# Performance work log

Measured on AMD Instinct MI355X. Metric: run time of the kernel, lower is better.

## Reference

```python
import jax, jax.numpy as jnp
import numpy as np

B, S, D = 4, 2048, 1024      # batch, seq, d_model
H = 4096                     # expert hidden_size
E, K = 8, 2                  # num_experts, top_k
Z_COEF, BAL_COEF = 0.001, 0.01


def setup_inputs() -> dict:
    key = jax.random.key(0)
    ks = jax.random.split(key, 10)
    sc = 0.02
    return {
        "x": jax.random.normal(ks[0], (B, S, D), jnp.float32),
        "gate_w": jax.random.normal(ks[1], (D, E), jnp.float32) * sc,
        "keys_w": jax.random.normal(ks[2], (E, D, H), jnp.float32) * sc,
        "keys_b": jnp.zeros((E, H), jnp.float32),
        "values_w": jax.random.normal(ks[3], (E, H, D), jnp.float32) * sc,
        "values_b": jnp.zeros((E, D), jnp.float32),
        "shared_keys_w": jax.random.normal(ks[4], (D, H), jnp.float32) * sc,
        "shared_keys_b": jnp.zeros((H,), jnp.float32),
        "shared_values_w": jax.random.normal(ks[5], (H, D), jnp.float32) * sc,
        "shared_values_b": jnp.zeros((D,), jnp.float32),
    }


def reference(x, gate_w, keys_w, keys_b, values_w, values_b,
              shared_keys_w, shared_keys_b, shared_values_w, shared_values_b):
    b, s, d = x.shape
    xf = x.reshape(-1, d)                                  # [N, D]

    # ---- Router (top-k, softmax over selected scores) ----
    logits = xf @ gate_w                                   # [N, E]
    scores, idx = jax.lax.top_k(logits, K)                 # [N, K]
    w = jax.nn.softmax(scores, axis=-1)                    # [N, K]

    # Aux losses (training path)
    one_hot = jax.nn.one_hot(idx, E, dtype=w.dtype)        # [N, K, E]
    usage = (one_hot * w[..., None]).sum(axis=(0, 1))      # [E]
    balance_loss = usage.std() / usage.mean() * BAL_COEF
    z_loss = jnp.square(jax.nn.logsumexp(logits, axis=-1)).mean() * Z_COEF
    router_loss = balance_loss + z_loss

    # ---- Shared expert(s): single FFN, divided by count (=1) ----
    out = jax.nn.gelu(xf @ shared_keys_w + shared_keys_b) @ shared_values_w + shared_values_b

    # ---- Training path: dense per-expert FFN, masked combine ----
    # hidden: [N, E, H]
    hidden = jax.nn.gelu(jnp.einsum('nd,edh->neh', xf, keys_w) + keys_b)
    expert_out = jnp.einsum('neh,ehd->ned', hidden, values_w) + values_b  # [N, E, D]
    comb = (one_hot * w[..., None]).sum(axis=1)            # [N, E] per-token expert weight
    out = out + jnp.einsum('ned,ne->nd', expert_out, comb)

    return out.reshape(b, s, d), router_loss
```

## Files before the change

kernel.cpp:

```cpp
#include <hip/hip_runtime.h>
#include <hip/hip_bf16.h>


#define N_TOK 8192
#define DM    1024
#define HD    4096
#define NE    8
#define NKTOT 16384
#define PERM_CAP 17408
#define MAX_TILES 136
#define BAND 17
#define EV_BLOCKS 1088
#define RTOK_BLK 16

typedef __attribute__((ext_vector_type(8))) short bhalf8;
typedef __attribute__((ext_vector_type(8))) unsigned short ushort8v;
typedef __attribute__((ext_vector_type(4))) float floatx4;

__device__ __forceinline__ unsigned short f2bf(float f) {
  union { float f; unsigned int u; } v; v.f = f;
  unsigned int u = v.u;
  return (unsigned short)((u + 0x7fffu + ((u >> 16) & 1u)) >> 16);
}

__device__ __forceinline__ float bf2f(unsigned short h) {
  union { unsigned int u; float f; } v; v.u = ((unsigned int)h) << 16;
  return v.f;
}

__device__ __forceinline__ float gelu_tanh(float h) {
  float u = 0.7978845608028654f * (h + 0.044715f * h * h * h);
  float t = 1.0f - 2.0f / (1.0f + __expf(2.0f * u));
  return 0.5f * h * (1.0f + t);
}

__device__ __forceinline__ void gload16(const unsigned short* g, void* l) {
  __builtin_amdgcn_global_load_lds(
      (const __attribute__((address_space(1))) void*)g,
      (__attribute__((address_space(3))) void*)l, 16, 0, 0);
}

__global__ void init_cvt_kernel(const float* __restrict__ x, unsigned short* __restrict__ xb,
                                int* perm, float* permw, float* usage, float* zsum,
                                int* counts, int* fill) {
  int b = blockIdx.x;
  int i = b * 256 + threadIdx.x;
  size_t ci = (size_t)i * 4;
  float4 v = *(const float4*)(x + ci);
  ushort4 o;
  o.x = f2bf(v.x); o.y = f2bf(v.y); o.z = f2bf(v.z); o.w = f2bf(v.w);
  *(ushort4*)(xb + ci) = o;
  if (i < PERM_CAP) { perm[i] = 0; permw[i] = 0.0f; }
  if (i < NE) { usage[i] = 0.0f; counts[i] = 0; fill[i] = 0; }
  if (i == 0) zsum[0] = 0.0f;
}

__global__ void router_kernel(const float* __restrict__ x, const float* __restrict__ gw,
                              int* __restrict__ idxb, float* __restrict__ wbuf,
                              float* __restrict__ usage, float* __restrict__ zsum,
                              int* __restrict__ counts) {
  __shared__ float s_use[NE];
  __shared__ int   s_cnt[NE];
  __shared__ float s_z;
  int t = threadIdx.x;
  if (t < NE) { s_use[t] = 0.0f; s_cnt[t] = 0; }
  if (t == 0) s_z = 0.0f;
  __syncthreads();

  int wave = t >> 6;
  int lane = t & 63;

  float luse[NE]; int lcnt[NE];
#pragma unroll
  for (int e = 0; e < NE; e++) { luse[e] = 0.0f; lcnt[e] = 0; }
  float lz = 0.0f;

#pragma unroll
  for (int i = 0; i < 4; i++) {
    int n = blockIdx.x * RTOK_BLK + wave * 4 + i;
    const float* xr = x + (size_t)n * DM;
    float acc[NE];
#pragma unroll
    for (int e = 0; e < NE; e++) acc[e] = 0.0f;
    for (int d = lane; d < DM; d += 64) {
      float xv = xr[d];
      const float* g = gw + (size_t)d * NE;
#pragma unroll
      for (int e = 0; e < NE; e++) acc[e] += xv * g[e];
    }
#pragma unroll
    for (int e = 0; e < NE; e++) {
#pragma unroll
      for (int off = 32; off > 0; off >>= 1) acc[e] += __shfl_xor(acc[e], off);
    }
    if (lane == 0) {
      float m1 = acc[0]; int i1 = 0;
#pragma unroll
      for (int e = 1; e < NE; e++) if (acc[e] > m1) { m1 = acc[e]; i1 = e; }
      float m2 = -3.0e38f; int i2 = 0;
#pragma unroll
      for (int e = 0; e < NE; e++) if (e != i1 && acc[e] > m2) { m2 = acc[e]; i2 = e; }
      float e1 = __expf(m2 - m1);
      float w1 = 1.0f / (1.0f + e1);
      float w2 = e1 / (1.0f + e1);
      float s = 0.0f;
#pragma unroll
      for (int e = 0; e < NE; e++) s += __expf(acc[e] - m1);
      float lse = m1 + __logf(s);
      idxb[n * 2 + 0] = i1; idxb[n * 2 + 1] = i2;
      wbuf[n * 2 + 0] = w1; wbuf[n * 2 + 1] = w2;
      luse[i1] += w1; luse[i2] += w2;
      lcnt[i1]++;     lcnt[i2]++;
      lz += lse * lse;
    }
  }

  if (lane == 0) {
#pragma unroll
    for (int e = 0; e < NE; e++) {
      atomicAdd(&s_use[e], luse[e]);
      atomicAdd(&s_cnt[e], lcnt[e]);
    }
    atomicAdd(&s_z, lz);
  }
  __syncthreads();
  if (t < NE) {
    atomicAdd(&usage[t], s_use[t]);
    atomicAdd(&counts[t], s_cnt[t]);
  }
  if (t == 0) atomicAdd(zsum, s_z);
}

__global__ void scan_kernel(const int* __restrict__ counts, int* __restrict__ poff,
                            int* __restrict__ tileE, int* __restrict__ tileR,
                            int* __restrict__ nTiles,
                            const float* __restrict__ usage, const float* __restrict__ zsum,
                            float* __restrict__ lossOut) {
  if (threadIdx.x == 0 && blockIdx.x == 0) {
    int run = 0, nt = 0;
    for (int e = 0; e < NE; e++) {
      poff[e] = run;
      int t = (counts[e] + 127) >> 7;
      for (int i = 0; i < t; i++) { tileE[nt] = e; tileR[nt] = run + i * 128; nt++; }
      run += t << 7;
    }
    *nTiles = nt;
    float mean = 0.0f;
    for (int e = 0; e < NE; e++) mean += usage[e];
    mean *= (1.0f / NE);
    float var = 0.0f;
    for (int e = 0; e < NE; e++) { float d = usage[e] - mean; var += d * d; }
    var *= (1.0f / NE);
    float bal = sqrtf(var) / mean * 0.01f;
    float z = (zsum[0] / (float)N_TOK) * 0.001f;
    lossOut[0] = bal + z;
  }
}

__global__ void scatter_kernel(const int* __restrict__ idxb, const float* __restrict__ wbuf,
                               const int* __restrict__ poff, int* __restrict__ fill,
                               int* __restrict__ perm, float* __restrict__ permw,
                               int* __restrict__ pos) {
  __shared__ int lcnt[NE];
  __shared__ int lbase[NE];
  int t = threadIdx.x;
  if (t < NE) lcnt[t] = 0;
  __syncthreads();
  int i = blockIdx.x * 256 + t;
  int e = idxb[i];
  int r = atomicAdd(&lcnt[e], 1);
  __syncthreads();
  if (t < NE) lbase[t] = atomicAdd(&fill[t], lcnt[t]);
  __syncthreads();
  int p = poff[e] + lbase[e] + r;
  perm[p] = i >> 1;
  permw[p] = wbuf[i];
  pos[i] = p;
}

__device__ __forceinline__ void tr_body(const float* __restrict__ src,
                                        unsigned short* __restrict__ dst, int R, int C) {
  __shared__ float tile[64][65];
  int r0 = blockIdx.x * 64, c0 = blockIdx.y * 64;
  int c = threadIdx.x & 63, r = threadIdx.x >> 6;
#pragma unroll
  for (int i = 0; i < 16; i++)
    tile[r + i * 4][c] = src[(size_t)(r0 + r + i * 4) * C + c0 + c];
  __syncthreads();
  int u = threadIdx.x & 7;
  int ow = threadIdx.x >> 3;
#pragma unroll
  for (int it = 0; it < 2; it++) {
    int oc = ow + it * 32;
    ushort8v o;
#pragma unroll
    for (int j = 0; j < 8; j++) o[j] = f2bf(tile[u * 8 + j][oc]);
    *(ushort8v*)&dst[(size_t)(c0 + oc) * R + r0 + u * 8] = o;
  }
}

__global__ void transpose_cvt9_kernel(const float* __restrict__ srcB,
                                      const float* __restrict__ src1,
                                      unsigned short* __restrict__ dstB,
                                      unsigned short* __restrict__ dst1, int R, int C) {
  int z = blockIdx.z;
  const float* src = (z < NE) ? srcB + (size_t)z * R * C : src1;
  unsigned short* dst = (z < NE) ? dstB + (size_t)z * R * C : dst1;
  tr_body(src, dst, R, C);
}

__global__ void combine_kernel(float* __restrict__ out,
                               const unsigned short* __restrict__ eout,
                               const int* __restrict__ pos) {
  int t = blockIdx.x;
  int d = threadIdx.x * 8;
  int p0 = pos[t * 2], p1 = pos[t * 2 + 1];
  float* o = out + (size_t)t * DM + d;
  const unsigned short* e0 = eout + (size_t)p0 * DM + d;
  const unsigned short* e1 = eout + (size_t)p1 * DM + d;
  float4 a = *(const float4*)(o);
  float4 b = *(const float4*)(o + 4);
  ushort4 u0a = *(const ushort4*)(e0), u0b = *(const ushort4*)(e0 + 4);
  ushort4 u1a = *(const ushort4*)(e1), u1b = *(const ushort4*)(e1 + 4);
  a.x += bf2f(u0a.x) + bf2f(u1a.x);
  a.y += bf2f(u0a.y) + bf2f(u1a.y);
  a.z += bf2f(u0a.z) + bf2f(u1a.z);
  a.w += bf2f(u0a.w) + bf2f(u1a.w);
  b.x += bf2f(u0b.x) + bf2f(u1b.x);
  b.y += bf2f(u0b.y) + bf2f(u1b.y);
  b.z += bf2f(u0b.z) + bf2f(u1b.z);
  b.w += bf2f(u0b.w) + bf2f(u1b.w);
  *(float4*)(o) = a;
  *(float4*)(o + 4) = b;
}

__global__ __launch_bounds__(256, 4) void gemm_expert_keys(
    const unsigned short* __restrict__ A, const unsigned short* __restrict__ BT,
    const float* __restrict__ bias, unsigned short* __restrict__ outH,
    int Kd, int Nd,
    const int* __restrict__ perm, const int* __restrict__ tileE,
    const int* __restrict__ tileR, const int* __restrict__ nTiles) {
  __shared__ __align__(16) unsigned short As[128 * 64];
  __shared__ __align__(16) unsigned short Bs[128 * 64];

  int id = blockIdx.x;
  int xcd = id & 7, q = id >> 3;
  int n_in = q & 7, m_in = (q >> 3) & 3, ng = (q >> 5) & 3, mg = q >> 7;
  int mband = mg * 4 + m_in;
  if (mband >= BAND) return;
  int mt = xcd * BAND + mband;
  int ntile = ng * 8 + n_in;
  if (mt >= *nTiles) return;
  int e = tileE[mt];
  int prow0 = tileR[mt];
  BT += (size_t)e * Kd * Nd;
  bias += (size_t)e * Nd;
  int n0 = ntile * 128;

  int t = threadIdx.x;
  int rsub = t >> 3;
  int gc = (t & 7) ^ (rsub & 7);
  const unsigned short* aptr[4];
  const unsigned short* bptr[4];
#pragma unroll
  for (int p = 0; p < 4; p++) {
    int r = rsub + p * 32;
    aptr[p] = A + (size_t)perm[prow0 + r] * Kd + gc * 8;
    bptr[p] = BT + (size_t)(n0 + r) * Kd + gc * 8;
  }
  char* ldsA = (char*)As + (t & 192) * 16;
  char* ldsB = (char*)Bs + (t & 192) * 16;

  int lane = t & 63;
  int wv = t >> 6;
  int wm = (wv >> 1) * 64, wn = (wv & 1) * 64;
  int lr = lane & 15, lq = lane >> 4;
  int rx = lr & 7;

  floatx4 acc[4][4];
#pragma unroll
  for (int i = 0; i < 4; i++)
#pragma unroll
    for (int j = 0; j < 4; j++) acc[i][j] = (floatx4){0.f, 0.f, 0.f, 0.f};

  for (int k0 = 0; k0 < Kd; k0 += 64) {
#pragma unroll
    for (int p = 0; p < 4; p++) {
      gload16(aptr[p] + k0, ldsA + p * 4096);
      gload16(bptr[p] + k0, ldsB + p * 4096);
    }
    __syncthreads();
#pragma unroll
    for (int kk = 0; kk < 2; kk++) {
      int ca = kk * 4 + lq;
      bhalf8 af[4], bf[4];
#pragma unroll
      for (int i = 0; i < 4; i++) {
        af[i] = *(const bhalf8*)&As[(wm + i * 16 + lr) * 64 + ((ca ^ rx) * 8)];
        bf[i] = *(const bhalf8*)&Bs[(wn + i * 16 + lr) * 64 + ((ca ^ rx) * 8)];
      }
#pragma unroll
      for (int mtile = 0; mtile < 4; mtile++)
#pragma unroll
        for (int ntl = 0; ntl < 4; ntl++)
          acc[mtile][ntl] = __builtin_amdgcn_mfma_f32_16x16x32_bf16(af[mtile], bf[ntl], acc[mtile][ntl], 0, 0, 0);
    }
    __syncthreads();
  }

#pragma unroll
  for (int mtile = 0; mtile < 4; mtile++) {
#pragma unroll
    for (int ntl = 0; ntl < 4; ntl++) {
      int ncol = n0 + wn + ntl * 16 + lr;
      float bb = bias[ncol];
#pragma unroll
      for (int r = 0; r < 4; r++) {
        int mrow = wm + mtile * 16 + lq * 4 + r;
        float v = acc[mtile][ntl][r] + bb;
        outH[(size_t)(prow0 + mrow) * Nd + ncol] = f2bf(gelu_tanh(v));
      }
    }
  }
}

__global__ __launch_bounds__(256, 4) void gemm_shared_values(
    const unsigned short* __restrict__ A, const unsigned short* __restrict__ BT,
    const float* __restrict__ bias, float* __restrict__ outF) {
  __shared__ __align__(16) unsigned short As[128 * 64];
  __shared__ __align__(16) unsigned short Bs[64 * 64];

  int id = blockIdx.x;
  int xcd = id & 7, q = id >> 3;
  int mt = xcd * 8 + (q >> 4);
  int ntile = q & 15;
  int m0 = mt * 128, n0 = ntile * 64;

  int t = threadIdx.x;
  int rsub = t >> 3;
  int gc = (t & 7) ^ (rsub & 7);
  const unsigned short* aptr[4];
  const unsigned short* bptr[2];
#pragma unroll
  for (int p = 0; p < 4; p++)
    aptr[p] = A + (size_t)(m0 + rsub + p * 32) * HD + gc * 8;
#pragma unroll
  for (int p = 0; p < 2; p++)
    bptr[p] = BT + (size_t)(n0 + rsub + p * 32) * HD + gc * 8;
  char* ldsA = (char*)As + (t & 192) * 16;
  char* ldsB = (char*)Bs + (t & 192) * 16;

  int lane = t & 63;
  int wv = t >> 6;
  int wm = (wv >> 1) * 64, wn = (wv & 1) * 32;
  int lr = lane & 15, lq = lane >> 4;
  int rx = lr & 7;

  floatx4 acc[4][2];
#pragma unroll
  for (int i = 0; i < 4; i++)
#pragma unroll
    for (int j = 0; j < 2; j++) acc[i][j] = (floatx4){0.f, 0.f, 0.f, 0.f};

  for (int k0 = 0; k0 < HD; k0 += 64) {
#pragma unroll
    for (int p = 0; p < 4; p++) gload16(aptr[p] + k0, ldsA + p * 4096);
#pragma unroll
    for (int p = 0; p < 2; p++) gload16(bptr[p] + k0, ldsB + p * 4096);
    __syncthreads();
#pragma unroll
    for (int kk = 0; kk < 2; kk++) {
      int ca = kk * 4 + lq;
      bhalf8 af[4], bf[2];
#pragma unroll
      for (int i = 0; i < 4; i++)
        af[i] = *(const bhalf8*)&As[(wm + i * 16 + lr) * 64 + ((ca ^ rx) * 8)];
#pragma unroll
      for (int j = 0; j < 2; j++)
        bf[j] = *(const bhalf8*)&Bs[(wn + j * 16 + lr) * 64 + ((ca ^ rx) * 8)];
#pragma unroll
      for (int i = 0; i < 4; i++)
#pragma unroll
        for (int j = 0; j < 2; j++)
          acc[i][j] = __builtin_amdgcn_mfma_f32_16x16x32_bf16(af[i], bf[j], acc[i][j], 0, 0, 0);
    }
    __syncthreads();
  }

#pragma unroll
  for (int i = 0; i < 4; i++) {
#pragma unroll
    for (int j = 0; j < 2; j++) {
      int ncol = n0 + wn + j * 16 + lr;
      float bb = bias[ncol];
#pragma unroll
      for (int r = 0; r < 4; r++) {
        int mrow = m0 + wm + i * 16 + lq * 4 + r;
        outF[(size_t)mrow * DM + ncol] = acc[i][j][r] + bb;
      }
    }
  }
}

__global__ __launch_bounds__(256, 4) void gemm_ev_sk(
    const unsigned short* __restrict__ hid, const unsigned short* __restrict__ wtV,
    const float* __restrict__ values_b, unsigned short* __restrict__ eout,
    const unsigned short* __restrict__ xb, const unsigned short* __restrict__ wtK8,
    const float* __restrict__ sk_b, unsigned short* __restrict__ hidS,
    const float* __restrict__ permw,
    const int* __restrict__ tileE, const int* __restrict__ tileR,
    const int* __restrict__ nTiles) {
  __shared__ __align__(16) unsigned short As[128 * 64];
  __shared__ __align__(16) unsigned short Bs[128 * 64];

  int id = blockIdx.x;
  bool is_ev = id < EV_BLOCKS;

  int Kd, rbase, n0;
  const unsigned short* A;
  const unsigned short* BT;
  const float* bias;
  if (is_ev) {
    int xcd = id & 7, q = id >> 3;
    int mt = xcd * BAND + (q >> 3);
    if (mt >= *nTiles) return;
    int e = tileE[mt];
    rbase = tileR[mt];
    n0 = (q & 7) * 128;
    Kd = HD;
    A = hid;
    BT = wtV + (size_t)e * HD * DM;
    bias = values_b + (size_t)e * DM;
  } else {
    int id2 = id - EV_BLOCKS;
    int xcd = id2 & 7, q = id2 >> 3;
    int mt = xcd * 8 + (q & 7);
    rbase = mt * 128;
    n0 = (q >> 3) * 128;
    Kd = DM;
    A = xb;
    BT = wtK8;
    bias = sk_b;
  }

  int t = threadIdx.x;
  int rsub = t >> 3;
  int gc = (t & 7) ^ (rsub & 7);
  const unsigned short* aptr[4];
  const unsigned short* bptr[4];
#pragma unroll
  for (int p = 0; p < 4; p++) {
    int r = rsub + p * 32;
    aptr[p] = A + (size_t)(rbase + r) * Kd + gc * 8;
    bptr[p] = BT + (size_t)(n0 + r) * Kd + gc * 8;
  }
  char* ldsA = (char*)As + (t & 192) * 16;
  char* ldsB = (char*)Bs + (t & 192) * 16;

  int lane = t & 63;
  int wv = t >> 6;
  int wm = (wv >> 1) * 64, wn = (wv & 1) * 64;
  int lr = lane & 15, lq = lane >> 4;
  int rx = lr & 7;

  floatx4 acc[4][4];
#pragma unroll
  for (int i = 0; i < 4; i++)
#pragma unroll
    for (int j = 0; j < 4; j++) acc[i][j] = (floatx4){0.f, 0.f, 0.f, 0.f};

  for (int k0 = 0; k0 < Kd; k0 += 64) {
#pragma unroll
    for (int p = 0; p < 4; p++) {
      gload16(aptr[p] + k0, ldsA + p * 4096);
      gload16(bptr[p] + k0, ldsB + p * 4096);
    }
    __syncthreads();
#pragma unroll
    for (int kk = 0; kk < 2; kk++) {
      int ca = kk * 4 + lq;
      bhalf8 af[4], bf[4];
#pragma unroll
      for (int i = 0; i < 4; i++) {
        af[i] = *(const bhalf8*)&As[(wm + i * 16 + lr) * 64 + ((ca ^ rx) * 8)];
        bf[i] = *(const bhalf8*)&Bs[(wn + i * 16 + lr) * 64 + ((ca ^ rx) * 8)];
      }
#pragma unroll
      for (int mtile = 0; mtile < 4; mtile++)
#pragma unroll
        for (int ntl = 0; ntl < 4; ntl++)
          acc[mtile][ntl] = __builtin_amdgcn_mfma_f32_16x16x32_bf16(af[mtile], bf[ntl], acc[mtile][ntl], 0, 0, 0);
    }
    __syncthreads();
  }

  if (is_ev) {
#pragma unroll
    for (int mtile = 0; mtile < 4; mtile++) {
#pragma unroll
      for (int ntl = 0; ntl < 4; ntl++) {
        int ncol = n0 + wn + ntl * 16 + lr;
        float bb = bias[ncol];
#pragma unroll
        for (int r = 0; r < 4; r++) {
          int prow = rbase + wm + mtile * 16 + lq * 4 + r;
          float w = permw[prow];
          float v = acc[mtile][ntl][r] + bb;
          eout[(size_t)prow * DM + ncol] = f2bf(w * v);
        }
      }
    }
  } else {
#pragma unroll
    for (int mtile = 0; mtile < 4; mtile++) {
#pragma unroll
      for (int ntl = 0; ntl < 4; ntl++) {
        int ncol = n0 + wn + ntl * 16 + lr;
        float bb = bias[ncol];
#pragma unroll
        for (int r = 0; r < 4; r++) {
          int mrow = rbase + wm + mtile * 16 + lq * 4 + r;
          float v = acc[mtile][ntl][r] + bb;
          hidS[(size_t)mrow * HD + ncol] = f2bf(gelu_tanh(v));
        }
      }
    }
  }
}

extern "C" void kernel_launch(void* const* d_in, const int* in_sizes, int n_in,
                              void* d_out, int out_size, void* d_ws, size_t ws_size,
                              hipStream_t stream) {
  const float* x        = (const float*)d_in[0];
  const float* gate_w   = (const float*)d_in[1];
  const float* keys_w   = (const float*)d_in[2];
  const float* keys_b   = (const float*)d_in[3];
  const float* values_w = (const float*)d_in[4];
  const float* values_b = (const float*)d_in[5];
  const float* sk_w     = (const float*)d_in[6];
  const float* sk_b     = (const float*)d_in[7];
  const float* sv_w     = (const float*)d_in[8];
  const float* sv_b     = (const float*)d_in[9];
  float* out = (float*)d_out;

  char* p = (char*)d_ws;
  unsigned short* xb   = (unsigned short*)p; p += (size_t)N_TOK * DM * 2;
  unsigned short* wt   = (unsigned short*)p; p += (size_t)(NE + 2) * DM * HD * 2;
  unsigned short* hid  = (unsigned short*)p; p += (size_t)(PERM_CAP + N_TOK) * HD * 2;
  unsigned short* eout = (unsigned short*)p; p += (size_t)PERM_CAP * DM * 2;
  int*   idxb   = (int*)p;   p += NKTOT * 4;
  float* wbuf   = (float*)p; p += NKTOT * 4;
  int*   perm   = (int*)p;   p += PERM_CAP * 4;
  float* permw  = (float*)p; p += PERM_CAP * 4;
  int*   pos    = (int*)p;   p += NKTOT * 4;
  int*   counts = (int*)p;   p += NE * 4;
  int*   fill   = (int*)p;   p += NE * 4;
  int*   poff   = (int*)p;   p += NE * 4;
  float* usage  = (float*)p; p += NE * 4;
  float* zsum   = (float*)p; p += 16;
  int*   tileE  = (int*)p;   p += MAX_TILES * 4;
  int*   tileR  = (int*)p;   p += MAX_TILES * 4;
  int*   nTiles = (int*)p;   p += 16;

  float* lossOut = out + (size_t)N_TOK * DM;
  unsigned short* wt8  = wt + (size_t)NE * DM * HD;
  unsigned short* wt9  = wt + (size_t)(NE + 1) * DM * HD;
  unsigned short* hidS = hid + (size_t)PERM_CAP * HD;

  init_cvt_kernel<<<N_TOK * DM / 4 / 256, 256, 0, stream>>>(
      x, xb, perm, permw, usage, zsum, counts, fill);
  router_kernel<<<N_TOK / RTOK_BLK, 256, 0, stream>>>(x, gate_w, idxb, wbuf, usage, zsum, counts);
  scan_kernel<<<1, 64, 0, stream>>>(counts, poff, tileE, tileR, nTiles, usage, zsum, lossOut);
  scatter_kernel<<<NKTOT / 256, 256, 0, stream>>>(idxb, wbuf, poff, fill, perm, permw, pos);

  transpose_cvt9_kernel<<<dim3(DM / 64, HD / 64, NE + 1), 256, 0, stream>>>(
      keys_w, sk_w, wt, wt8, DM, HD);

  gemm_expert_keys<<<5120, 256, 0, stream>>>(
      xb, wt, keys_b, hid, DM, HD, perm, tileE, tileR, nTiles);

  transpose_cvt9_kernel<<<dim3(HD / 64, DM / 64, NE + 1), 256, 0, stream>>>(
      values_w, sv_w, wt, wt9, HD, DM);
  gemm_ev_sk<<<EV_BLOCKS + 2048, 256, 0, stream>>>(
      hid, wt, values_b, eout, xb, wt8, sk_b, hidS,
      permw, tileE, tileR, nTiles);

  gemm_shared_values<<<1024, 256, 0, stream>>>(hidS, wt9, sv_b, out);

  combine_kernel<<<N_TOK, 128, 0, stream>>>(out, eout, pos);
}
```

Before: 890.3 us.

## Fold weight transposes into router and expert-keys GEMM launches for overlap

The keys-weight transpose/convert now runs as extra blocks inside the router launch, and the values-weight transpose runs as extra blocks appended to the expert-keys GEMM launch. This removes two separate kernel launches and lets the bandwidth-bound transposes overlap with the router and GEMM work on idle CUs. Separate wtK/wtV buffers are used so the values transpose no longer overwrites keys weights that the same launch still reads. The cost is a larger workspace and transpose blocks that may contend with GEMM blocks for memory bandwidth and CU slots.

Measured after the change: 1.028 ms. +15.5%, slower.

```diff
diff --git a/kernel.cpp b/kernel.cpp
--- a/kernel.cpp
+++ b/kernel.cpp
@@ -11,6 +11,9 @@
 #define MAX_TILES 136
 #define BAND 17
 #define EV_BLOCKS 1088
+#define EK_BLOCKS 5120
+#define RTR_BLOCKS 512
+#define TR_BLOCKS 9216
 #define RTOK_BLK 16
 
 typedef __attribute__((ext_vector_type(8))) short bhalf8;
@@ -40,11 +43,32 @@
       (__attribute__((address_space(3))) void*)l, 16, 0, 0);
 }
 
+__device__ __forceinline__ void tr_body_p(float (*tile)[65],
+                                          const float* __restrict__ src,
+                                          unsigned short* __restrict__ dst,
+                                          int R, int C, int bx, int by) {
+  int r0 = bx * 64, c0 = by * 64;
+  int c = threadIdx.x & 63, r = threadIdx.x >> 6;
+#pragma unroll
+  for (int i = 0; i < 16; i++)
+    tile[r + i * 4][c] = src[(size_t)(r0 + r + i * 4) * C + c0 + c];
+  __syncthreads();
+  int u = threadIdx.x & 7;
+  int ow = threadIdx.x >> 3;
+#pragma unroll
+  for (int it = 0; it < 2; it++) {
+    int oc = ow + it * 32;
+    ushort8v o;
+#pragma unroll
+    for (int j = 0; j < 8; j++) o[j] = f2bf(tile[u * 8 + j][oc]);
+    *(ushort8v*)&dst[(size_t)(c0 + oc) * R + r0 + u * 8] = o;
+  }
+}
+
 __global__ void init_cvt_kernel(const float* __restrict__ x, unsigned short* __restrict__ xb,
                                 int* perm, float* permw, float* usage, float* zsum,
                                 int* counts, int* fill) {
-  int b = blockIdx.x;
-  int i = b * 256 + threadIdx.x;
+  int i = blockIdx.x * 256 + threadIdx.x;
   size_t ci = (size_t)i * 4;
   float4 v = *(const float4*)(x + ci);
   ushort4 o;
@@ -55,14 +79,28 @@
   if (i == 0) zsum[0] = 0.0f;
 }
 
-__global__ void router_kernel(const float* __restrict__ x, const float* __restrict__ gw,
-                              int* __restrict__ idxb, float* __restrict__ wbuf,
-                              float* __restrict__ usage, float* __restrict__ zsum,
-                              int* __restrict__ counts) {
+__global__ void router_keystr_kernel(
+    const float* __restrict__ x, const float* __restrict__ gw,
+    int* __restrict__ idxb, float* __restrict__ wbuf,
+    float* __restrict__ usage, float* __restrict__ zsum, int* __restrict__ counts,
+    const float* __restrict__ keys_w, const float* __restrict__ sk_w,
+    unsigned short* __restrict__ wtK) {
+  __shared__ float tile[64][65];
   __shared__ float s_use[NE];
   __shared__ int   s_cnt[NE];
   __shared__ float s_z;
+
+  int id = blockIdx.x;
   int t = threadIdx.x;
+  if (id >= RTR_BLOCKS) {
+    int tt = id - RTR_BLOCKS;
+    int bx = tt & 15, by = (tt >> 4) & 63, z = tt >> 10;
+    const float* src = (z < NE) ? keys_w + (size_t)z * DM * HD : sk_w;
+    unsigned short* dst = wtK + (size_t)z * DM * HD;
+    tr_body_p(tile, src, dst, DM, HD, bx, by);
+    return;
+  }
+
   if (t < NE) { s_use[t] = 0.0f; s_cnt[t] = 0; }
   if (t == 0) s_z = 0.0f;
   __syncthreads();
@@ -77,7 +115,7 @@
 
 #pragma unroll
   for (int i = 0; i < 4; i++) {
-    int n = blockIdx.x * RTOK_BLK + wave * 4 + i;
+    int n = id * RTOK_BLK + wave * 4 + i;
     const float* xr = x + (size_t)n * DM;
     float acc[NE];
 #pragma unroll
@@ -176,37 +214,6 @@
   perm[p] = i >> 1;
   permw[p] = wbuf[i];
   pos[i] = p;
-}
-
-__device__ __forceinline__ void tr_body(const float* __restrict__ src,
-                                        unsigned short* __restrict__ dst, int R, int C) {
-  __shared__ float tile[64][65];
-  int r0 = blockIdx.x * 64, c0 = blockIdx.y * 64;
-  int c = threadIdx.x & 63, r = threadIdx.x >> 6;
-#pragma unroll
-  for (int i = 0; i < 16; i++)
-    tile[r + i * 4][c] = src[(size_t)(r0 + r + i * 4) * C + c0 + c];
-  __syncthreads();
-  int u = threadIdx.x & 7;
-  int ow = threadIdx.x >> 3;
-#pragma unroll
-  for (int it = 0; it < 2; it++) {
-    int oc = ow + it * 32;
-    ushort8v o;
-#pragma unroll
-    for (int j = 0; j < 8; j++) o[j] = f2bf(tile[u * 8 + j][oc]);
-    *(ushort8v*)&dst[(size_t)(c0 + oc) * R + r0 + u * 8] = o;
-  }
-}
-
-__global__ void transpose_cvt9_kernel(const float* __restrict__ srcB,
-                                      const float* __restrict__ src1,
-                                      unsigned short* __restrict__ dstB,
-                                      unsigned short* __restrict__ dst1, int R, int C) {
-  int z = blockIdx.z;
-  const float* src = (z < NE) ? srcB + (size_t)z * R * C : src1;
-  unsigned short* dst = (z < NE) ? dstB + (size_t)z * R * C : dst1;
-  tr_body(src, dst, R, C);
 }
 
 __global__ void combine_kernel(float* __restrict__ out,
@@ -234,16 +241,27 @@
   *(float4*)(o + 4) = b;
 }
 
-__global__ __launch_bounds__(256, 4) void gemm_expert_keys(
-    const unsigned short* __restrict__ A, const unsigned short* __restrict__ BT,
+__global__ __launch_bounds__(256, 4) void gemm_ek_vtr(
+    const unsigned short* __restrict__ A, const unsigned short* __restrict__ wtK,
     const float* __restrict__ bias, unsigned short* __restrict__ outH,
-    int Kd, int Nd,
     const int* __restrict__ perm, const int* __restrict__ tileE,
-    const int* __restrict__ tileR, const int* __restrict__ nTiles) {
-  __shared__ __align__(16) unsigned short As[128 * 64];
-  __shared__ __align__(16) unsigned short Bs[128 * 64];
+    const int* __restrict__ tileR, const int* __restrict__ nTiles,
+    const float* __restrict__ values_w, const float* __restrict__ sv_w,
+    unsigned short* __restrict__ wtV) {
+  __shared__ __align__(16) char shbuf[32768];
+  unsigned short* As = (unsigned short*)shbuf;
+  unsigned short* Bs = (unsigned short*)(shbuf + 16384);
 
   int id = blockIdx.x;
+  if (id >= EK_BLOCKS) {
+    int tt = id - EK_BLOCKS;
+    int bx = tt & 63, by = (tt >> 6) & 15, z = tt >> 10;
+    const float* src = (z < NE) ? values_w + (size_t)z * HD * DM : sv_w;
+    unsigned short* dst = wtV + (size_t)z * HD * DM;
+    tr_body_p((float(*)[65])shbuf, src, dst, HD, DM, bx, by);
+    return;
+  }
+
   int xcd = id & 7, q = id >> 3;
   int n_in = q & 7, m_in = (q >> 3) & 3, ng = (q >> 5) & 3, mg = q >> 7;
   int mband = mg * 4 + m_in;
@@ -253,8 +271,8 @@
   if (mt >= *nTiles) return;
   int e = tileE[mt];
   int prow0 = tileR[mt];
-  BT += (size_t)e * Kd * Nd;
-  bias += (size_t)e * Nd;
+  const unsigned short* BT = wtK + (size_t)e * DM * HD;
+  const float* be = bias + (size_t)e * HD;
   int n0 = ntile * 128;
 
   int t = threadIdx.x;
@@ -265,11 +283,11 @@
 #pragma unroll
   for (int p = 0; p < 4; p++) {
     int r = rsub + p * 32;
-    aptr[p] = A + (size_t)perm[prow0 + r] * Kd + gc * 8;
-    bptr[p] = BT + (size_t)(n0 + r) * Kd + gc * 8;
-  }
-  char* ldsA = (char*)As + (t & 192) * 16;
-  char* ldsB = (char*)Bs + (t & 192) * 16;
+    aptr[p] = A + (size_t)perm[prow0 + r] * DM + gc * 8;
+    bptr[p] = BT + (size_t)(n0 + r) * DM + gc * 8;
+  }
+  char* ldsA = shbuf + (t & 192) * 16;
+  char* ldsB = shbuf + 16384 + (t & 192) * 16;
 
   int lane = t & 63;
   int wv = t >> 6;
@@ -283,7 +301,7 @@
 #pragma unroll
     for (int j = 0; j < 4; j++) acc[i][j] = (floatx4){0.f, 0.f, 0.f, 0.f};
 
-  for (int k0 = 0; k0 < Kd; k0 += 64) {
+  for (int k0 = 0; k0 < DM; k0 += 64) {
 #pragma unroll
     for (int p = 0; p < 4; p++) {
       gload16(aptr[p] + k0, ldsA + p * 4096);
@@ -313,12 +331,12 @@
 #pragma unroll
     for (int ntl = 0; ntl < 4; ntl++) {
       int ncol = n0 + wn + ntl * 16 + lr;
-      float bb = bias[ncol];
+      float bb = be[ncol];
 #pragma unroll
       for (int r = 0; r < 4; r++) {
         int mrow = wm + mtile * 16 + lq * 4 + r;
         float v = acc[mtile][ntl][r] + bb;
-        outH[(size_t)(prow0 + mrow) * Nd + ncol] = f2bf(gelu_tanh(v));
+        outH[(size_t)(prow0 + mrow) * HD + ncol] = f2bf(gelu_tanh(v));
       }
     }
   }
@@ -545,7 +563,8 @@
 
   char* p = (char*)d_ws;
   unsigned short* xb   = (unsigned short*)p; p += (size_t)N_TOK * DM * 2;
-  unsigned short* wt   = (unsigned short*)p; p += (size_t)(NE + 2) * DM * HD * 2;
+  unsigned short* wtK  = (unsigned short*)p; p += (size_t)(NE + 1) * DM * HD * 2;
+  unsigned short* wtV  = (unsigned short*)p; p += (size_t)(NE + 1) * DM * HD * 2;
   unsigned short* hid  = (unsigned short*)p; p += (size_t)(PERM_CAP + N_TOK) * HD * 2;
   unsigned short* eout = (unsigned short*)p; p += (size_t)PERM_CAP * DM * 2;
   int*   idxb   = (int*)p;   p += NKTOT * 4;
@@ -563,29 +582,24 @@
   int*   nTiles = (int*)p;   p += 16;
 
   float* lossOut = out + (size_t)N_TOK * DM;
-  unsigned short* wt8  = wt + (size_t)NE * DM * HD;
-  unsigned short* wt9  = wt + (size_t)(NE + 1) * DM * HD;
+  unsigned short* wtK8 = wtK + (size_t)NE * DM * HD;
+  unsigned short* wtV8 = wtV + (size_t)NE * DM * HD;
   unsigned short* hidS = hid + (size_t)PERM_CAP * HD;
 
   init_cvt_kernel<<<N_TOK * DM / 4 / 256, 256, 0, stream>>>(
       x, xb, perm, permw, usage, zsum, counts, fill);
-  router_kernel<<<N_TOK / RTOK_BLK, 256, 0, stream>>>(x, gate_w, idxb, wbuf, usage, zsum, counts);
+  router_keystr_kernel<<<RTR_BLOCKS + TR_BLOCKS, 256, 0, stream>>>(
+      x, gate_w, idxb, wbuf, usage, zsum, counts, keys_w, sk_w, wtK);
   scan_kernel<<<1, 64, 0, stream>>>(counts, poff, tileE, tileR, nTiles, usage, zsum, lossOut);
   scatter_kernel<<<NKTOT / 256, 256, 0, stream>>>(idxb, wbuf, poff, fill, perm, permw, pos);
 
-  transpose_cvt9_kernel<<<dim3(DM / 64, HD / 64, NE + 1), 256, 0, stream>>>(
-      keys_w, sk_w, wt, wt8, DM, HD);
-
-  gemm_expert_keys<<<5120, 256, 0, stream>>>(
-      xb, wt, keys_b, hid, DM, HD, perm, tileE, tileR, nTiles);
-
-  transpose_cvt9_kernel<<<dim3(HD / 64, DM / 64, NE + 1), 256, 0, stream>>>(
-      values_w, sv_w, wt, wt9, HD, DM);
+  gemm_ek_vtr<<<EK_BLOCKS + TR_BLOCKS, 256, 0, stream>>>(
+      xb, wtK, keys_b, hid, perm, tileE, tileR, nTiles, values_w, sv_w, wtV);
+
   gemm_ev_sk<<<EV_BLOCKS + 2048, 256, 0, stream>>>(
-      hid, wt, values_b, eout, xb, wt8, sk_b, hidS,
+      hid, wtV, values_b, eout, xb, wtK8, sk_b, hidS,
       permw, tileE, tileR, nTiles);
 
-  gemm_shared_values<<<1024, 256, 0, stream>>>(hidS, wt9, sv_b, out);
-
+  gemm_shared_values<<<1024, 256, 0, stream>>>(hidS, wtV8, sv_b, out);
   combine_kernel<<<N_TOK, 128, 0, stream>>>(out, eout, pos);
 }
```
